# Kernel tuning notes

Measured on AMD Instinct MI355X. Metric: run time of the kernel, lower is better.

The kernel has to match this reference:

```python
import jax, jax.numpy as jnp
import numpy as np

B, K = 4096, 64
D_MODEL, D_DYN, D_STAT = 256, 512, 64
H = 4
DH = D_MODEL // H
SCALE = DH ** -0.5
LN_EPS = 1e-5


def _ln(x, g, b):
    m = x.mean(-1, keepdims=True)
    v = ((x - m) ** 2).mean(-1, keepdims=True)
    return (x - m) * jax.lax.rsqrt(v + LN_EPS) * g + b


def setup_inputs() -> dict:
    key = jax.random.key(0)
    ks = jax.random.split(key, 16)
    w = lambda k, s: jax.random.normal(k, s, jnp.float32) * 0.02
    return {
        "h_dyn": jax.random.normal(ks[0], (B, D_DYN), jnp.float32),
        "x_stat": jax.random.normal(ks[1], (B, K, D_STAT), jnp.float32),
        "W_dyn": w(ks[2], (D_DYN, D_MODEL)), "b_dyn": jnp.zeros((D_MODEL,)),
        "W_stat": w(ks[3], (D_STAT, D_MODEL)), "b_stat": jnp.zeros((D_MODEL,)),
        "g_ndyn": jnp.ones((D_MODEL,)), "b_ndyn": jnp.zeros((D_MODEL,)),
        "g_nstat": jnp.ones((D_MODEL,)), "b_nstat": jnp.zeros((D_MODEL,)),
        "Wq": w(ks[4], (D_MODEL, D_MODEL)), "bq": jnp.zeros((D_MODEL,)),
        "Wk": w(ks[5], (D_MODEL, D_MODEL)), "bk": jnp.zeros((D_MODEL,)),
        "Wv": w(ks[6], (D_MODEL, D_MODEL)), "bv": jnp.zeros((D_MODEL,)),
        "g_mlp": jnp.ones((D_MODEL,)), "b_mlp": jnpp if False else jnp.zeros((D_MODEL,)),
        "W1": w(ks[7], (D_MODEL, D_MODEL)), "b1": jnp.zeros((D_MODEL,)),
        "W2": w(ks[8], (D_MODEL, D_MODEL)), "b2": jnp.zeros((D_MODEL,)),
        "Wo": w(ks[9], (D_MODEL, D_MODEL)), "bo": jnp.zeros((D_MODEL,)),
        "res_scale": jnp.float32(0.1),
    }


def reference(h_dyn, x_stat, W_dyn, b_dyn, W_stat, b_stat, g_ndyn, b_ndyn,
              g_nstat, b_nstat, Wq, bq, Wk, bk, Wv, bv, g_mlp, b_mlp,
              W1, b1, W2, b2, Wo, bo, res_scale):
    h0 = h_dyn @ W_dyn + b_dyn                  # [B, d_model]
    s = x_stat @ W_stat + b_stat                # [B, K, d_model]
    h = _ln(h0, g_ndyn, b_ndyn)
    s = _ln(s, g_nstat, b_nstat)

    q = (h @ Wq + bq).reshape(B, H, DH)         # [B, H, dh]
    k = (s @ Wk + bk).reshape(B, K, H, DH)      # [B, K, H, dh]
    v_flat = s @ Wv + bv                        # [B, K, d_model]

    # per-variable MLP (DeepSets style): LN -> Linear -> GELU(exact) -> Linear
    t = _ln(v_flat, g_mlp, b_mlp)
    t = jax.nn.gelu(t @ W1 + b1, approximate=False)
    v_tokens = t @ W2 + b2                      # [B, K, d_model]

    logits = jnp.einsum('bhd,bkhd->bhk', q, k) * SCALE   # [B, H, K]
    w = jax.nn.sigmoid(logits)
    w = w / (w.sum(-1, keepdims=True) + 1e-6)

    vh = v_tokens.reshape(B, K, H, DH)
    z = jnp.einsum('bhk,bkhd->bhd', w, vh).reshape(B, D_MODEL)
    c = z @ Wo + bo
    c = h0 + res_scale * c
    w_mean = w.mean(axis=1)                     # [B, K]
    return c, w_mean
```

## Files before the change

### kernel.cpp

```cpp
#include <hip/hip_runtime.h>
#include <cmath>


typedef __bf16 bf16;
typedef bf16 bf16x4 __attribute__((ext_vector_type(4)));
typedef bf16 bf16x8 __attribute__((ext_vector_type(8)));
typedef float f32x4 __attribute__((ext_vector_type(4)));

#define MFMA_B16(a, b, c) __builtin_amdgcn_mfma_f32_16x16x32_bf16((a), (b), (c), 0, 0, 0)
#define RCP(x) __builtin_amdgcn_rcpf(x)
#define RSQ(x) __builtin_amdgcn_rsqf(x)

constexpr int SROW = 264;
constexpr int XROW = 72;

constexpr size_t WSTAT_P = 0;
constexpr size_t WV_P    = 16384;
constexpr size_t W1_P    = 81920;
constexpr size_t W2O_P   = 147456;
constexpr size_t WDYN_P  = 212992;
constexpr size_t WQ_P    = 344064;
constexpr size_t WK_P    = 409600;
constexpr size_t KQ_BF   = 475136;
constexpr size_t H0_F   = 2334720;
constexpr size_t BKQ_F  = 3383296;
constexpr size_t B2O_F  = 3399680;
constexpr size_t W2OS_F = 3399936;

__device__ __forceinline__ bf16x8 zero8() {
  bf16x8 z;
#pragma unroll
  for (int j = 0; j < 8; ++j) z[j] = (bf16)0.0f;
  return z;
}

__device__ __forceinline__ float wave_sum(float v) {
#pragma unroll
  for (int m = 1; m < 64; m <<= 1) v += __shfl_xor(v, m, 64);
  return v;
}

__device__ __forceinline__ void zero_acc(f32x4 (&acc)[4][4]) {
#pragma unroll
  for (int mt = 0; mt < 4; ++mt)
#pragma unroll
    for (int nt = 0; nt < 4; ++nt) { f32x4 z = {0.f, 0.f, 0.f, 0.f}; acc[mt][nt] = z; }
}

__device__ __forceinline__ void gemm_swapped_p(const bf16* buf, const bf16* __restrict__ Wp,
                                               int w, int lane, int l16, int koff,
                                               f32x4 (&acc)[4][4]) {
  const bf16* base = Wp + (size_t)w * 8 * 2048 + lane * 8;
  bf16x8 aw[2][4];
#pragma unroll
  for (int dt = 0; dt < 4; ++dt) aw[0][dt] = *(const bf16x8*)(base + dt * 512);
#pragma unroll
  for (int ks = 0; ks < 8; ++ks) {
    const int cur = ks & 1;
    if (ks < 7) {
#pragma unroll
      for (int dt = 0; dt < 4; ++dt)
        aw[cur ^ 1][dt] = *(const bf16x8*)(base + (ks + 1) * 2048 + dt * 512);
    }
#pragma unroll
    for (int tt = 0; tt < 4; ++tt) {
      bf16x8 bfrag = *(const bf16x8*)(buf + (tt * 16 + l16) * SROW + ks * 32 + koff);
#pragma unroll
      for (int dt = 0; dt < 4; ++dt) acc[dt][tt] = MFMA_B16(aw[cur][dt], bfrag, acc[dt][tt]);
    }
  }
}

__device__ __forceinline__ void gemm_orig_p(const bf16* buf, const bf16* __restrict__ Wp,
                                            int w, int lane, int l16, int koff,
                                            f32x4 (&acc)[4][4]) {
  const bf16* base = Wp + (size_t)w * 8 * 2048 + lane * 8;
  bf16x8 bw[2][4];
#pragma unroll
  for (int nt = 0; nt < 4; ++nt) bw[0][nt] = *(const bf16x8*)(base + nt * 512);
#pragma unroll
  for (int ks = 0; ks < 8; ++ks) {
    const int cur = ks & 1;
    if (ks < 7) {
#pragma unroll
      for (int nt = 0; nt < 4; ++nt)
        bw[cur ^ 1][nt] = *(const bf16x8*)(base + (ks + 1) * 2048 + nt * 512);
    }
#pragma unroll
    for (int mt = 0; mt < 4; ++mt) {
      bf16x8 a = *(const bf16x8*)(buf + (mt * 16 + l16) * SROW + ks * 32 + koff);
#pragma unroll
      for (int nt = 0; nt < 4; ++nt) acc[mt][nt] = MFMA_B16(a, bw[cur][nt], acc[mt][nt]);
    }
  }
}

__device__ __forceinline__ void bias_stats(f32x4 (&acc)[4][4], const float* __restrict__ bsrc,
                                           int w, int quad, int l16,
                                           float (*part_s)[64], float (*part_ss)[64]) {
  float ps[4] = {0.f, 0.f, 0.f, 0.f}, pq[4] = {0.f, 0.f, 0.f, 0.f};
#pragma unroll
  for (int dt = 0; dt < 4; ++dt) {
    const float4 bb = *(const float4*)(bsrc + w * 64 + dt * 16 + quad * 4);
#pragma unroll
    for (int tt = 0; tt < 4; ++tt) {
      float v0 = acc[dt][tt][0] + bb.x;
      float v1 = acc[dt][tt][1] + bb.y;
      float v2 = acc[dt][tt][2] + bb.z;
      float v3 = acc[dt][tt][3] + bb.w;
      acc[dt][tt][0] = v0; acc[dt][tt][1] = v1; acc[dt][tt][2] = v2; acc[dt][tt][3] = v3;
      ps[tt] += (v0 + v1) + (v2 + v3);
      pq[tt] += v0 * v0 + v1 * v1 + v2 * v2 + v3 * v3;
    }
  }
#pragma unroll
  for (int tt = 0; tt < 4; ++tt) {
    ps[tt] += __shfl_xor(ps[tt], 16, 64); ps[tt] += __shfl_xor(ps[tt], 32, 64);
    pq[tt] += __shfl_xor(pq[tt], 16, 64); pq[tt] += __shfl_xor(pq[tt], 32, 64);
  }
  if (quad == 0) {
#pragma unroll
    for (int tt = 0; tt < 4; ++tt) {
      part_s[w][tt * 16 + l16] = ps[tt];
      part_ss[w][tt * 16 + l16] = pq[tt];
    }
  }
}

__device__ __forceinline__ void ln_apply_store(f32x4 (&acc)[4][4], const float* __restrict__ g,
                                               const float* __restrict__ bsh, bf16* buf,
                                               const float (*part_s)[64],
                                               const float (*part_ss)[64],
                                               int w, int quad, int l16) {
  float mean[4], rstd[4];
#pragma unroll
  for (int tt = 0; tt < 4; ++tt) {
    const int tok = tt * 16 + l16;
    float s = (part_s[0][tok] + part_s[1][tok]) + (part_s[2][tok] + part_s[3][tok]);
    float q = (part_ss[0][tok] + part_ss[1][tok]) + (part_ss[2][tok] + part_ss[3][tok]);
    mean[tt] = s * (1.f / 256.f);
    float var = q * (1.f / 256.f) - mean[tt] * mean[tt];
    rstd[tt] = RSQ(var + 1e-5f);
  }
#pragma unroll
  for (int dt = 0; dt < 4; ++dt) {
    const float4 gv = *(const float4*)(g + w * 64 + dt * 16 + quad * 4);
    const float4 bv = *(const float4*)(bsh + w * 64 + dt * 16 + quad * 4);
#pragma unroll
    for (int tt = 0; tt < 4; ++tt) {
      float t0 = (acc[dt][tt][0] - mean[tt]) * rstd[tt];
      float t1 = (acc[dt][tt][1] - mean[tt]) * rstd[tt];
      float t2 = (acc[dt][tt][2] - mean[tt]) * rstd[tt];
      float t3 = (acc[dt][tt][3] - mean[tt]) * rstd[tt];
      bf16x4 o;
      o[0] = (bf16)(t0 * gv.x + bv.x);
      o[1] = (bf16)(t1 * gv.y + bv.y);
      o[2] = (bf16)(t2 * gv.z + bv.z);
      o[3] = (bf16)(t3 * gv.w + bv.w);
      *(bf16x4*)(buf + (tt * 16 + l16) * SROW + w * 64 + dt * 16 + quad * 4) = o;
    }
  }
}

__device__ __forceinline__ void pack_slice(const float* __restrict__ src, bf16* __restrict__ dstb,
                                           int w, int ks, bool trans, float* sh, int tid) {
  if (!trans) {
#pragma unroll
    for (int i = 0; i < 8; ++i) {
      int r = i * 4 + (tid >> 6), c = tid & 63;
      sh[r * 65 + c] = src[(size_t)(ks * 32 + r) * 256 + w * 64 + c];
    }
  } else {
    int c = tid >> 2, j8 = tid & 3;
#pragma unroll
    for (int jj = 0; jj < 8; ++jj) {
      int r = j8 * 8 + jj;
      sh[r * 65 + c] = src[(size_t)(w * 64 + c) * 256 + ks * 32 + r];
    }
  }
  __syncthreads();
  const int x = tid >> 6, quad = (tid >> 4) & 3, l16 = tid & 15;
  bf16x8 o;
#pragma unroll
  for (int j = 0; j < 8; ++j) o[j] = (bf16)sh[(quad * 8 + j) * 65 + x * 16 + l16];
  *(bf16x8*)(dstb + tid * 8) = o;
}

__global__ void prep1_kernel(const float* __restrict__ Wdyn, const float* __restrict__ Wstat,
                             const float* __restrict__ Wq, const float* __restrict__ Wk,
                             const float* __restrict__ Wv, const float* __restrict__ W1,
                             const float* __restrict__ W2, const float* __restrict__ Wo,
                             const float* __restrict__ b2,
                             bf16* __restrict__ ws, float* __restrict__ wsf) {
  __shared__ float sh[64 * 65];
  __shared__ float part[4][8];
  const int idx = blockIdx.x;
  const int tid = threadIdx.x;

  if (idx < 32) {
    const int n0 = idx * 8;
    float4 a0 = *(const float4*)(Wo + (size_t)tid * 256 + n0);
    float4 a1 = *(const float4*)(Wo + (size_t)tid * 256 + n0 + 4);
    sh[tid * 8 + 0] = a0.x; sh[tid * 8 + 1] = a0.y; sh[tid * 8 + 2] = a0.z; sh[tid * 8 + 3] = a0.w;
    sh[tid * 8 + 4] = a1.x; sh[tid * 8 + 5] = a1.y; sh[tid * 8 + 6] = a1.z; sh[tid * 8 + 7] = a1.w;
    __syncthreads();
    float acc[8] = {0.f, 0.f, 0.f, 0.f, 0.f, 0.f, 0.f, 0.f};
    const float* row = W2 + (size_t)tid * 256;
    for (int d0 = 0; d0 < 256; d0 += 4) {
      float4 wv = *(const float4*)(row + d0);
#pragma unroll
      for (int dd = 0; dd < 4; ++dd) {
        float r = (dd == 0) ? wv.x : (dd == 1) ? wv.y : (dd == 2) ? wv.z : wv.w;
        const float* cc = &sh[(d0 + dd) * 8];
#pragma unroll
        for (int j = 0; j < 8; ++j) acc[j] += r * cc[j];
      }
    }
    float* dst = wsf + W2OS_F;
#pragma unroll
    for (int j = 0; j < 8; ++j) dst[(size_t)tid * 256 + n0 + j] = acc[j];
    const int w = tid >> 6, lane = tid & 63;
    float bval = b2[tid];
#pragma unroll
    for (int j = 0; j < 8; ++j) {
      float p = wave_sum(bval * sh[tid * 8 + j]);
      if (lane == 0) part[w][j] = p;
    }
    __syncthreads();
    if (tid < 8)
      wsf[B2O_F + n0 + tid] = part[0][tid] + part[1][tid] + part[2][tid] + part[3][tid];
    return;
  }

  int t = idx - 32;
  const float* src; bf16* dst; int KS; bool trans = false;
  if (t < 64)       { src = Wdyn;  dst = ws + WDYN_P;  KS = 16; }
  else if (t < 72)  { src = Wstat; dst = ws + WSTAT_P; KS = 2;  t -= 64; }
  else if (t < 104) { src = Wq;    dst = ws + WQ_P;    KS = 8;  t -= 72; }
  else if (t < 136) { src = Wv;    dst = ws + WV_P;    KS = 8;  t -= 104; }
  else if (t < 168) { src = W1;    dst = ws + W1_P;    KS = 8;  t -= 136; }
  else              { src = Wk;    dst = ws + WK_P;    KS = 8;  t -= 168; trans = true; }
  const int w = t / KS, ks = t % KS;
  pack_slice(src, dst + (size_t)(w * KS + ks) * 2048, w, ks, trans, sh, tid);
}

__global__ void prep2_kernel(const float* __restrict__ wsf_scr, bf16* __restrict__ ws) {
  __shared__ float sh[64 * 65];
  const int t = blockIdx.x;
  pack_slice(wsf_scr, ws + W2O_P + (size_t)t * 2048, t >> 3, t & 7, false, sh, threadIdx.x);
}

__launch_bounds__(256, 2)
__global__ void pre_kernel(const float* __restrict__ h_dyn, const float* __restrict__ b_dyn,
                           const float* __restrict__ g_ndyn, const float* __restrict__ b_ndyn,
                           const float* __restrict__ bq, const float* __restrict__ bk,
                           const bf16* __restrict__ Wdyn_p, const bf16* __restrict__ Wq_p,
                           const bf16* __restrict__ Wk_p,
                           float* __restrict__ h0_out, bf16* __restrict__ kq_out,
                           float* __restrict__ bkq_out) {
  __shared__ float h0t[8][264];
  __shared__ bf16 hlnt[8][264];
  __shared__ bf16 qt[8][264];
  const int tid = threadIdx.x;
  const int w = tid >> 6, lane = tid & 63, quad = lane >> 4, l16 = lane & 15;
  const int koff = quad * 8;
  const int b0 = blockIdx.x * 8;
  const int mrow = l16 & 7;

  {
    f32x4 acc[4];
#pragma unroll
    for (int nt = 0; nt < 4; ++nt) { f32x4 z = {0.f, 0.f, 0.f, 0.f}; acc[nt] = z; }
    const float* arow = h_dyn + (size_t)(b0 + mrow) * 512;
    const bf16* base = Wdyn_p + (size_t)w * 16 * 2048 + lane * 8;
    bf16x8 bw[2][4];
#pragma unroll
    for (int nt = 0; nt < 4; ++nt) bw[0][nt] = *(const bf16x8*)(base + nt * 512);
    for (int ks = 0; ks < 16; ++ks) {
      const int cur = ks & 1;
      if (ks < 15) {
#pragma unroll
        for (int nt = 0; nt < 4; ++nt)
          bw[cur ^ 1][nt] = *(const bf16x8*)(base + (ks + 1) * 2048 + nt * 512);
      }
      float4 x0 = *(const float4*)(arow + ks * 32 + koff);
      float4 x1 = *(const float4*)(arow + ks * 32 + koff + 4);
      bf16x8 a;
      a[0] = (bf16)x0.x; a[1] = (bf16)x0.y; a[2] = (bf16)x0.z; a[3] = (bf16)x0.w;
      a[4] = (bf16)x1.x; a[5] = (bf16)x1.y; a[6] = (bf16)x1.z; a[7] = (bf16)x1.w;
#pragma unroll
      for (int nt = 0; nt < 4; ++nt) acc[nt] = MFMA_B16(a, bw[cur][nt], acc[nt]);
    }
    if (quad < 2) {
#pragma unroll
      for (int nt = 0; nt < 4; ++nt) {
        int col = w * 64 + nt * 16 + l16;
        float bb = b_dyn[col];
#pragma unroll
        for (int r = 0; r < 4; ++r) {
          int row = quad * 4 + r;
          float v = acc[nt][r] + bb;
          h0t[row][col] = v;
          h0_out[(size_t)(b0 + row) * 256 + col] = v;
        }
      }
    }
  }
  __syncthreads();

  {
    float gn[4], bn[4];
#pragma unroll
    for (int j = 0; j < 4; ++j) { gn[j] = g_ndyn[lane + 64 * j]; bn[j] = b_ndyn[lane + 64 * j]; }
#pragma unroll
    for (int i = 0; i < 2; ++i) {
      int row = 4 * i + w;
      float x[4]; float s = 0.f, ss = 0.f;
#pragma unroll
      for (int j = 0; j < 4; ++j) { x[j] = h0t[row][lane + 64 * j]; s += x[j]; ss += x[j] * x[j]; }
      s = wave_sum(s); ss = wave_sum(ss);
      float mean = s * (1.f / 256.f);
      float var = ss * (1.f / 256.f) - mean * mean;
      float rstd = RSQ(var + 1e-5f);
#pragma unroll
      for (int j = 0; j < 4; ++j)
        hlnt[row][lane + 64 * j] = (bf16)((x[j] - mean) * rstd * gn[j] + bn[j]);
    }
  }
  __syncthreads();

  {
    f32x4 acc[4];
#pragma unroll
    for (int nt = 0; nt < 4; ++nt) { f32x4 z = {0.f, 0.f, 0.f, 0.f}; acc[nt] = z; }
    const bf16* base = Wq_p + (size_t)w * 8 * 2048 + lane * 8;
    bf16x8 bw[2][4];
#pragma unroll
    for (int nt = 0; nt < 4; ++nt) bw[0][nt] = *(const bf16x8*)(base + nt * 512);
    for (int ks = 0; ks < 8; ++ks) {
      const int cur = ks & 1;
      if (ks < 7) {
#pragma unroll
        for (int nt = 0; nt < 4; ++nt)
          bw[cur ^ 1][nt] = *(const bf16x8*)(base + (ks + 1) * 2048 + nt * 512);
      }
      bf16x8 a = *(const bf16x8*)(&hlnt[mrow][ks * 32 + koff]);
#pragma unroll
      for (int nt = 0; nt < 4; ++nt) acc[nt] = MFMA_B16(a, bw[cur][nt], acc[nt]);
    }
    if (quad < 2) {
#pragma unroll
      for (int nt = 0; nt < 4; ++nt) {
        int col = w * 64 + nt * 16 + l16;
        float bb = bq[col];
#pragma unroll
        for (int r = 0; r < 4; ++r)
          qt[quad * 4 + r][col] = (bf16)(acc[nt][r] + bb);
      }
    }
  }
  __syncthreads();

  {
    const int pair = tid >> 2;
    const int row = pair >> 2, h = pair & 3, sub = tid & 3;
    if (row < 8) {
      float p = 0.f;
#pragma unroll
      for (int j = 0; j < 16; ++j) {
        int e = sub * 16 + j;
        p += (float)qt[row][h * 64 + e] * bk[h * 64 + e];
      }
      p += __shfl_xor(p, 1, 64);
      p += __shfl_xor(p, 2, 64);
      if (sub == 0) bkq_out[(size_t)(b0 + row) * 4 + h] = p;
    }
  }

  for (int h = 0; h < 4; ++h) {
    f32x4 acc[4];
#pragma unroll
    for (int nt = 0; nt < 4; ++nt) { f32x4 z = {0.f, 0.f, 0.f, 0.f}; acc[nt] = z; }
    const bf16* base = Wk_p + (size_t)w * 8 * 2048 + lane * 8;
#pragma unroll
    for (int ks = 0; ks < 2; ++ks) {
      bf16x8 a = *(const bf16x8*)(&qt[mrow][h * 64 + ks * 32 + koff]);
#pragma unroll
      for (int nt = 0; nt < 4; ++nt) {
        bf16x8 bw = *(const bf16x8*)(base + (h * 2 + ks) * 2048 + nt * 512);
        acc[nt] = MFMA_B16(a, bw, acc[nt]);
      }
    }
    if (quad < 2) {
#pragma unroll
      for (int nt = 0; nt < 4; ++nt)
#pragma unroll
        for (int r = 0; r < 4; ++r)
          kq_out[(size_t)(b0 + quad * 4 + r) * 1024 + h * 256 + w * 64 + nt * 16 + l16] =
              (bf16)acc[nt][r];
    }
  }
}

__launch_bounds__(256, 4)
__global__ void fused_kernel(
    const float* __restrict__ x_stat, const float* __restrict__ b_stat,
    const float* __restrict__ g_nstat, const float* __restrict__ b_nstat,
    const float* __restrict__ bv, const float* __restrict__ g_mlp,
    const float* __restrict__ b_mlp, const float* __restrict__ b1,
    const float* __restrict__ bo, const float* __restrict__ res_scale_p,
    const float* __restrict__ h0g, const float* __restrict__ bkq_g,
    const float* __restrict__ b2o_g,
    const bf16* __restrict__ Wstat_p, const bf16* __restrict__ Wv_p,
    const bf16* __restrict__ W1_p, const bf16* __restrict__ W2o_p,
    const bf16* __restrict__ kq_g,
    float* __restrict__ out_c, float* __restrict__ out_wm) {

  __shared__ bf16 buf[64 * SROW];
  __shared__ float part_s[4][64];
  __shared__ float part_ss[4][64];
  __shared__ float watt[4][64];
  __shared__ float swh[4];

  const int b = blockIdx.x;
  const int tid = threadIdx.x;
  const int w = tid >> 6, lane = tid & 63, quad = lane >> 4, l16 = lane & 15;
  const int koff = quad * 8;

  bf16* xs = buf;
  {
    const float* xb = x_stat + (size_t)b * 4096;
#pragma unroll
    for (int j = 0; j < 4; ++j) {
      int idx = j * 1024 + tid * 4;
      float4 v = *(const float4*)(xb + idx);
      bf16x4 o;
      o[0] = (bf16)v.x; o[1] = (bf16)v.y; o[2] = (bf16)v.z; o[3] = (bf16)v.w;
      *(bf16x4*)(xs + (idx >> 6) * XROW + (idx & 63)) = o;
    }
  }
  __syncthreads();

  {
    f32x4 acc[4][4];
    zero_acc(acc);
    const bf16* wsb = Wstat_p + (size_t)w * 2 * 2048 + lane * 8;
    bf16x8 aw[2][4];
#pragma unroll
    for (int ks = 0; ks < 2; ++ks)
#pragma unroll
      for (int dt = 0; dt < 4; ++dt)
        aw[ks][dt] = *(const bf16x8*)(wsb + ks * 2048 + dt * 512);
#pragma unroll
    for (int ks = 0; ks < 2; ++ks)
#pragma unroll
      for (int tt = 0; tt < 4; ++tt) {
        bf16x8 bfrag = *(const bf16x8*)(xs + (tt * 16 + l16) * XROW + ks * 32 + koff);
#pragma unroll
        for (int dt = 0; dt < 4; ++dt) acc[dt][tt] = MFMA_B16(aw[ks][dt], bfrag, acc[dt][tt]);
      }
    bias_stats(acc, b_stat, w, quad, l16, part_s, part_ss);
    __syncthreads();
    ln_apply_store(acc, g_nstat, b_nstat, buf, part_s, part_ss, w, quad, l16);
  }
  __syncthreads();

  {
    const bf16* kq_b = kq_g + (size_t)b * 1024;
    f32x4 accL = {0.f, 0.f, 0.f, 0.f};
#pragma unroll
    for (int ks = 0; ks < 8; ++ks) {
      bf16x8 a = *(const bf16x8*)(buf + (w * 16 + l16) * SROW + ks * 32 + koff);
      bf16x8 kf = zero8();
      if (l16 < 4) kf = *(const bf16x8*)(kq_b + l16 * 256 + ks * 32 + koff);
      accL = MFMA_B16(a, kf, accL);
    }
    float bkqv = (l16 < 4) ? bkq_g[(size_t)b * 4 + l16] : 0.f;
#pragma unroll
    for (int r = 0; r < 4; ++r) {
      float lg = (accL[r] + bkqv) * 0.125f;
      float sig = RCP(1.f + __expf(-lg));
      if (l16 < 4) watt[l16][w * 16 + quad * 4 + r] = sig;
    }
  }

  {
    f32x4 acc[4][4];
    zero_acc(acc);
    gemm_swapped_p(buf, Wv_p, w, lane, l16, koff, acc);
    bias_stats(acc, bv, w, quad, l16, part_s, part_ss);
    __syncthreads();
    {
      float v = watt[w][lane];
      float den = wave_sum(v);
      float dinv = RCP(den + 1e-6f);
      watt[w][lane] = v * dinv;
      if (lane == 0) swh[w] = den * dinv;
    }
    ln_apply_store(acc, g_mlp, b_mlp, buf, part_s, part_ss, w, quad, l16);
  }
  __syncthreads();

  if (tid < 64)
    out_wm[(size_t)b * 64 + tid] =
        0.25f * ((watt[0][tid] + watt[1][tid]) + (watt[2][tid] + watt[3][tid]));

  {
    f32x4 acc[4][4];
    zero_acc(acc);
    gemm_swapped_p(buf, W1_p, w, lane, l16, koff, acc);
    __syncthreads();
#pragma unroll
    for (int dt = 0; dt < 4; ++dt) {
      const float4 bb = *(const float4*)(b1 + w * 64 + dt * 16 + quad * 4);
#pragma unroll
      for (int tt = 0; tt < 4; ++tt) {
        float v0 = acc[dt][tt][0] + bb.x;
        float v1 = acc[dt][tt][1] + bb.y;
        float v2 = acc[dt][tt][2] + bb.z;
        float v3 = acc[dt][tt][3] + bb.w;
        bf16x4 o;
        o[0] = (bf16)(v0 * RCP(1.f + __expf(-1.702f * v0)));
        o[1] = (bf16)(v1 * RCP(1.f + __expf(-1.702f * v1)));
        o[2] = (bf16)(v2 * RCP(1.f + __expf(-1.702f * v2)));
        o[3] = (bf16)(v3 * RCP(1.f + __expf(-1.702f * v3)));
        *(bf16x4*)(buf + (tt * 16 + l16) * SROW + w * 64 + dt * 16 + quad * 4) = o;
      }
    }
  }
  __syncthreads();

  {
    f32x4 acc[4][4];
    zero_acc(acc);
    gemm_orig_p(buf, W2o_p, w, lane, l16, koff, acc);
    float zacc[4] = {0.f, 0.f, 0.f, 0.f};
#pragma unroll
    for (int mt = 0; mt < 4; ++mt)
#pragma unroll
      for (int r = 0; r < 4; ++r) {
        float wt = watt[w][mt * 16 + quad * 4 + r];
#pragma unroll
        for (int nt = 0; nt < 4; ++nt) zacc[nt] += wt * acc[mt][nt][r];
      }
#pragma unroll
    for (int nt = 0; nt < 4; ++nt) {
      zacc[nt] += __shfl_xor(zacc[nt], 16, 64);
      zacc[nt] += __shfl_xor(zacc[nt], 32, 64);
    }
    if (quad == 0) {
      float rs = *res_scale_p;
#pragma unroll
      for (int nt = 0; nt < 4; ++nt) {
        int col = w * 64 + nt * 16 + l16;
        float res = zacc[nt] + swh[w] * b2o_g[col] + bo[col];
        out_c[(size_t)b * 256 + col] = h0g[(size_t)b * 256 + col] + rs * res;
      }
    }
  }
}

extern "C" void kernel_launch(void* const* d_in, const int* in_sizes, int n_in,
                              void* d_out, int out_size, void* d_ws, size_t ws_size,
                              hipStream_t stream) {
  const float* h_dyn   = (const float*)d_in[0];
  const float* x_stat  = (const float*)d_in[1];
  const float* W_dyn   = (const float*)d_in[2];
  const float* b_dyn   = (const float*)d_in[3];
  const float* W_stat  = (const float*)d_in[4];
  const float* b_stat  = (const float*)d_in[5];
  const float* g_ndyn  = (const float*)d_in[6];
  const float* b_ndyn  = (const float*)d_in[7];
  const float* g_nstat = (const float*)d_in[8];
  const float* b_nstat = (const float*)d_in[9];
  const float* Wq = (const float*)d_in[10];
  const float* bq = (const float*)d_in[11];
  const float* Wk = (const float*)d_in[12];
  const float* bk = (const float*)d_in[13];
  const float* Wv = (const float*)d_in[14];
  const float* bv = (const float*)d_in[15];
  const float* g_mlp = (const float*)d_in[16];
  const float* b_mlp = (const float*)d_in[17];
  const float* W1 = (const float*)d_in[18];
  const float* b1 = (const float*)d_in[19];
  const float* W2 = (const float*)d_in[20];
  const float* b2 = (const float*)d_in[21];
  const float* Wo = (const float*)d_in[22];
  const float* bo = (const float*)d_in[23];
  const float* rs = (const float*)d_in[24];

  bf16* ws = (bf16*)d_ws;
  float* wsf = (float*)d_ws;

  prep1_kernel<<<232, 256, 0, stream>>>(W_dyn, W_stat, Wq, Wk, Wv, W1, W2, Wo, b2, ws, wsf);
  prep2_kernel<<<32, 256, 0, stream>>>(wsf + W2OS_F, ws);

  pre_kernel<<<512, 256, 0, stream>>>(h_dyn, b_dyn, g_ndyn, b_ndyn, bq, bk,
                                      ws + WDYN_P, ws + WQ_P, ws + WK_P,
                                      wsf + H0_F, ws + KQ_BF, wsf + BKQ_F);

  float* out_c = (float*)d_out;
  float* out_wm = out_c + (size_t)4096 * 256;
  fused_kernel<<<4096, 256, 0, stream>>>(
      x_stat, b_stat, g_nstat, b_nstat, bv, g_mlp, b_mlp, b1, bo, rs,
      wsf + H0_F, wsf + BKQ_F, wsf + B2O_F,
      ws + WSTAT_P, ws + WV_P, ws + W1_P, ws + W2O_P, ws + KQ_BF,
      out_c, out_wm);
}
```

Measured before the change: 311.5 us.

## Replace precomputed W2·Wo fold with in-kernel W2 GEMM then Wo projection

Removes the prep kernel that computed the fused W2@Wo matrix and b2@Wo bias in fp32 and packed it separately. The fused kernel now runs the W2 GEMM in swapped orientation, reduces the attention-weighted tokens across lanes with shuffles, adds the weighted b2 bias, stages z in shared memory, and runs a small single-row MFMA against packed Wo. This drops one launch and a serial FP32 matmul in prep, at the cost of an extra sync, shuffle reductions and a mostly-zero MFMA pass per block in the main kernel.

```diff
diff --git a/kernel.cpp b/kernel.cpp
--- a/kernel.cpp
+++ b/kernel.cpp
@@ -17,15 +17,14 @@
 constexpr size_t WSTAT_P = 0;
 constexpr size_t WV_P    = 16384;
 constexpr size_t W1_P    = 81920;
-constexpr size_t W2O_P   = 147456;
-constexpr size_t WDYN_P  = 212992;
-constexpr size_t WQ_P    = 344064;
-constexpr size_t WK_P    = 409600;
-constexpr size_t KQ_BF   = 475136;
-constexpr size_t H0_F   = 2334720;
-constexpr size_t BKQ_F  = 3383296;
-constexpr size_t B2O_F  = 3399680;
-constexpr size_t W2OS_F = 3399936;
+constexpr size_t W2_P    = 147456;
+constexpr size_t WO_P    = 212992;
+constexpr size_t WDYN_P  = 278528;
+constexpr size_t WQ_P    = 409600;
+constexpr size_t WK_P    = 475136;
+constexpr size_t KQ_BF   = 540672;
+constexpr size_t H0_F  = 2367488;
+constexpr size_t BKQ_F = 3416064;
 
 __device__ __forceinline__ bf16x8 zero8() {
   bf16x8 z;
@@ -67,30 +66,6 @@
       bf16x8 bfrag = *(const bf16x8*)(buf + (tt * 16 + l16) * SROW + ks * 32 + koff);
 #pragma unroll
       for (int dt = 0; dt < 4; ++dt) acc[dt][tt] = MFMA_B16(aw[cur][dt], bfrag, acc[dt][tt]);
-    }
-  }
-}
-
-__device__ __forceinline__ void gemm_orig_p(const bf16* buf, const bf16* __restrict__ Wp,
-                                            int w, int lane, int l16, int koff,
-                                            f32x4 (&acc)[4][4]) {
-  const bf16* base = Wp + (size_t)w * 8 * 2048 + lane * 8;
-  bf16x8 bw[2][4];
-#pragma unroll
-  for (int nt = 0; nt < 4; ++nt) bw[0][nt] = *(const bf16x8*)(base + nt * 512);
-#pragma unroll
-  for (int ks = 0; ks < 8; ++ks) {
-    const int cur = ks & 1;
-    if (ks < 7) {
-#pragma unroll
-      for (int nt = 0; nt < 4; ++nt)
-        bw[cur ^ 1][nt] = *(const bf16x8*)(base + (ks + 1) * 2048 + nt * 512);
-    }
-#pragma unroll
-    for (int mt = 0; mt < 4; ++mt) {
-      bf16x8 a = *(const bf16x8*)(buf + (mt * 16 + l16) * SROW + ks * 32 + koff);
-#pragma unroll
-      for (int nt = 0; nt < 4; ++nt) acc[mt][nt] = MFMA_B16(a, bw[cur][nt], acc[mt][nt]);
     }
   }
 }
@@ -186,68 +161,24 @@
   *(bf16x8*)(dstb + tid * 8) = o;
 }
 
-__global__ void prep1_kernel(const float* __restrict__ Wdyn, const float* __restrict__ Wstat,
-                             const float* __restrict__ Wq, const float* __restrict__ Wk,
-                             const float* __restrict__ Wv, const float* __restrict__ W1,
-                             const float* __restrict__ W2, const float* __restrict__ Wo,
-                             const float* __restrict__ b2,
-                             bf16* __restrict__ ws, float* __restrict__ wsf) {
+__global__ void prep_kernel(const float* __restrict__ Wdyn, const float* __restrict__ Wstat,
+                            const float* __restrict__ Wq, const float* __restrict__ Wk,
+                            const float* __restrict__ Wv, const float* __restrict__ W1,
+                            const float* __restrict__ W2, const float* __restrict__ Wo,
+                            bf16* __restrict__ ws) {
   __shared__ float sh[64 * 65];
-  __shared__ float part[4][8];
-  const int idx = blockIdx.x;
-  const int tid = threadIdx.x;
-
-  if (idx < 32) {
-    const int n0 = idx * 8;
-    float4 a0 = *(const float4*)(Wo + (size_t)tid * 256 + n0);
-    float4 a1 = *(const float4*)(Wo + (size_t)tid * 256 + n0 + 4);
-    sh[tid * 8 + 0] = a0.x; sh[tid * 8 + 1] = a0.y; sh[tid * 8 + 2] = a0.z; sh[tid * 8 + 3] = a0.w;
-    sh[tid * 8 + 4] = a1.x; sh[tid * 8 + 5] = a1.y; sh[tid * 8 + 6] = a1.z; sh[tid * 8 + 7] = a1.w;
-    __syncthreads();
-    float acc[8] = {0.f, 0.f, 0.f, 0.f, 0.f, 0.f, 0.f, 0.f};
-    const float* row = W2 + (size_t)tid * 256;
-    for (int d0 = 0; d0 < 256; d0 += 4) {
-      float4 wv = *(const float4*)(row + d0);
-#pragma unroll
-      for (int dd = 0; dd < 4; ++dd) {
-        float r = (dd == 0) ? wv.x : (dd == 1) ? wv.y : (dd == 2) ? wv.z : wv.w;
-        const float* cc = &sh[(d0 + dd) * 8];
-#pragma unroll
-        for (int j = 0; j < 8; ++j) acc[j] += r * cc[j];
-      }
-    }
-    float* dst = wsf + W2OS_F;
-#pragma unroll
-    for (int j = 0; j < 8; ++j) dst[(size_t)tid * 256 + n0 + j] = acc[j];
-    const int w = tid >> 6, lane = tid & 63;
-    float bval = b2[tid];
-#pragma unroll
-    for (int j = 0; j < 8; ++j) {
-      float p = wave_sum(bval * sh[tid * 8 + j]);
-      if (lane == 0) part[w][j] = p;
-    }
-    __syncthreads();
-    if (tid < 8)
-      wsf[B2O_F + n0 + tid] = part[0][tid] + part[1][tid] + part[2][tid] + part[3][tid];
-    return;
-  }
-
-  int t = idx - 32;
+  int t = blockIdx.x;
   const float* src; bf16* dst; int KS; bool trans = false;
   if (t < 64)       { src = Wdyn;  dst = ws + WDYN_P;  KS = 16; }
   else if (t < 72)  { src = Wstat; dst = ws + WSTAT_P; KS = 2;  t -= 64; }
   else if (t < 104) { src = Wq;    dst = ws + WQ_P;    KS = 8;  t -= 72; }
   else if (t < 136) { src = Wv;    dst = ws + WV_P;    KS = 8;  t -= 104; }
   else if (t < 168) { src = W1;    dst = ws + W1_P;    KS = 8;  t -= 136; }
-  else              { src = Wk;    dst = ws + WK_P;    KS = 8;  t -= 168; trans = true; }
+  else if (t < 200) { src = W2;    dst = ws + W2_P;    KS = 8;  t -= 168; }
+  else if (t < 232) { src = Wo;    dst = ws + WO_P;    KS = 8;  t -= 200; }
+  else              { src = Wk;    dst = ws + WK_P;    KS = 8;  t -= 232; trans = true; }
   const int w = t / KS, ks = t % KS;
-  pack_slice(src, dst + (size_t)(w * KS + ks) * 2048, w, ks, trans, sh, tid);
-}
-
-__global__ void prep2_kernel(const float* __restrict__ wsf_scr, bf16* __restrict__ ws) {
-  __shared__ float sh[64 * 65];
-  const int t = blockIdx.x;
-  pack_slice(wsf_scr, ws + W2O_P + (size_t)t * 2048, t >> 3, t & 7, false, sh, threadIdx.x);
+  pack_slice(src, dst + (size_t)(w * KS + ks) * 2048, w, ks, trans, sh, threadIdx.x);
 }
 
 __launch_bounds__(256, 2)
@@ -408,12 +339,12 @@
     const float* __restrict__ g_nstat, const float* __restrict__ b_nstat,
     const float* __restrict__ bv, const float* __restrict__ g_mlp,
     const float* __restrict__ b_mlp, const float* __restrict__ b1,
-    const float* __restrict__ bo, const float* __restrict__ res_scale_p,
+    const float* __restrict__ b2, const float* __restrict__ bo,
+    const float* __restrict__ res_scale_p,
     const float* __restrict__ h0g, const float* __restrict__ bkq_g,
-    const float* __restrict__ b2o_g,
     const bf16* __restrict__ Wstat_p, const bf16* __restrict__ Wv_p,
-    const bf16* __restrict__ W1_p, const bf16* __restrict__ W2o_p,
-    const bf16* __restrict__ kq_g,
+    const bf16* __restrict__ W1_p, const bf16* __restrict__ W2_p,
+    const bf16* __restrict__ Wo_p, const bf16* __restrict__ kq_g,
     float* __restrict__ out_c, float* __restrict__ out_wm) {
 
   __shared__ bf16 buf[64 * SROW];
@@ -533,27 +464,61 @@
   {
     f32x4 acc[4][4];
     zero_acc(acc);
-    gemm_orig_p(buf, W2o_p, w, lane, l16, koff, acc);
-    float zacc[4] = {0.f, 0.f, 0.f, 0.f};
-#pragma unroll
-    for (int mt = 0; mt < 4; ++mt)
+    gemm_swapped_p(buf, W2_p, w, lane, l16, koff, acc);
+    float wt[4];
+#pragma unroll
+    for (int tt = 0; tt < 4; ++tt) wt[tt] = watt[w][tt * 16 + l16];
+    float zr[4][4];
+#pragma unroll
+    for (int dt = 0; dt < 4; ++dt)
 #pragma unroll
       for (int r = 0; r < 4; ++r) {
-        float wt = watt[w][mt * 16 + quad * 4 + r];
-#pragma unroll
-        for (int nt = 0; nt < 4; ++nt) zacc[nt] += wt * acc[mt][nt][r];
-      }
-#pragma unroll
-    for (int nt = 0; nt < 4; ++nt) {
-      zacc[nt] += __shfl_xor(zacc[nt], 16, 64);
-      zacc[nt] += __shfl_xor(zacc[nt], 32, 64);
+        float v = wt[0] * acc[dt][0][r] + wt[1] * acc[dt][1][r] +
+                  wt[2] * acc[dt][2][r] + wt[3] * acc[dt][3][r];
+        v += __shfl_xor(v, 1, 64);
+        v += __shfl_xor(v, 2, 64);
+        v += __shfl_xor(v, 4, 64);
+        v += __shfl_xor(v, 8, 64);
+        zr[dt][r] = v;
+      }
+    float* zs = &part_s[0][0];
+    if (l16 == 0) {
+      float sw = swh[w];
+#pragma unroll
+      for (int dt = 0; dt < 4; ++dt) {
+        const float4 b2v = *(const float4*)(b2 + w * 64 + dt * 16 + quad * 4);
+        float4 o;
+        o.x = zr[dt][0] + b2v.x * sw;
+        o.y = zr[dt][1] + b2v.y * sw;
+        o.z = zr[dt][2] + b2v.z * sw;
+        o.w = zr[dt][3] + b2v.w * sw;
+        *(float4*)(zs + w * 64 + dt * 16 + quad * 4) = o;
+      }
+    }
+    __syncthreads();
+    f32x4 a4[4];
+#pragma unroll
+    for (int nt = 0; nt < 4; ++nt) { f32x4 z = {0.f, 0.f, 0.f, 0.f}; a4[nt] = z; }
+    const bf16* base = Wo_p + (size_t)w * 8 * 2048 + lane * 8;
+#pragma unroll
+    for (int ks = 0; ks < 8; ++ks) {
+      bf16x8 a = zero8();
+      if (l16 == 0) {
+        float4 u0 = *(const float4*)(zs + ks * 32 + koff);
+        float4 u1 = *(const float4*)(zs + ks * 32 + koff + 4);
+        a[0] = (bf16)u0.x; a[1] = (bf16)u0.y; a[2] = (bf16)u0.z; a[3] = (bf16)u0.w;
+        a[4] = (bf16)u1.x; a[5] = (bf16)u1.y; a[6] = (bf16)u1.z; a[7] = (bf16)u1.w;
+      }
+#pragma unroll
+      for (int nt = 0; nt < 4; ++nt)
+        a4[nt] = MFMA_B16(a, *(const bf16x8*)(base + ks * 2048 + nt * 512), a4[nt]);
     }
     if (quad == 0) {
       float rs = *res_scale_p;
 #pragma unroll
       for (int nt = 0; nt < 4; ++nt) {
         int col = w * 64 + nt * 16 + l16;
-        float res = zacc[nt] + swh[w] * b2o_g[col] + bo[col];
+        float res = a4[nt][0] + bo[col];
         out_c[(size_t)b * 256 + col] = h0g[(size_t)b * 256 + col] + rs * res;
       }
     }
@@ -592,8 +557,7 @@
   bf16* ws = (bf16*)d_ws;
   float* wsf = (float*)d_ws;
 
-  prep1_kernel<<<232, 256, 0, stream>>>(W_dyn, W_stat, Wq, Wk, Wv, W1, W2, Wo, b2, ws, wsf);
-  prep2_kernel<<<32, 256, 0, stream>>>(wsf + W2OS_F, ws);
+  prep_kernel<<<264, 256, 0, stream>>>(W_dyn, W_stat, Wq, Wk, Wv, W1, W2, Wo, ws);
 
   pre_kernel<<<512, 256, 0, stream>>>(h_dyn, b_dyn, g_ndyn, b_ndyn, bq, bk,
                                       ws + WDYN_P, ws + WQ_P, ws + WK_P,
@@ -602,8 +566,8 @@
   float* out_c = (float*)d_out;
   float* out_wm = out_c + (size_t)4096 * 256;
   fused_kernel<<<4096, 256, 0, stream>>>(
-      x_stat, b_stat, g_nstat, b_nstat, bv, g_mlp, b_mlp, b1, bo, rs,
-      wsf + H0_F, wsf + BKQ_F, wsf + B2O_F,
-      ws + WSTAT_P, ws + WV_P, ws + W1_P, ws + W2O_P, ws + KQ_BF,
+      x_stat, b_stat, g_nstat, b_nstat, bv, g_mlp, b_mlp, b1, b2, bo, rs,
+      wsf + H0_F, wsf + BKQ_F,
+      ws + WSTAT_P, ws + WV_P, ws + W1_P, ws + W2_P, ws + WO_P, ws + KQ_BF,
       out_c, out_wm);
 }
```

Result: slower. 332.2 us (+6.6%).
